# Kernel optimization log

Measured on AMD Instinct MI355X. Metric: run time of the kernel, lower is better.

## Reference

```python
import jax, jax.numpy as jnp
import numpy as np

N_NODES = 100000
N_EDGES = 1600000
IN = 128
HID = 128
OUT_CLS = 40
EPS = 1e-12


def setup_inputs() -> dict:
    key = jax.random.key(0)
    ks = jax.random.split(key, 12)
    feat = jax.random.normal(ks[0], (N_NODES, IN), dtype=jnp.float32)
    edge_index = jax.random.randint(ks[1], (2, N_EDGES), 0, N_NODES, dtype=jnp.int64)

    def xavier(k, shape):
        fan_out, fan_in = shape
        lim = float(np.sqrt(6.0 / (fan_in + fan_out)))
        return jax.random.uniform(k, shape, jnp.float32, -lim, lim)

    return {
        "feat": feat,
        "edge_index": edge_index,
        "Wl1": xavier(ks[2], (HID, IN)),  "bl1": jnp.zeros((HID,), jnp.float32), "Wr1": xavier(ks[3], (HID, IN)),
        "Wl2": xavier(ks[4], (HID, HID)), "bl2": jnp.zeros((HID,), jnp.float32), "Wr2": xavier(ks[5], (HID, HID)),
        "Wl3": xavier(ks[6], (HID, HID)), "bl3": jnp.zeros((HID,), jnp.float32), "Wr3": xavier(ks[7], (HID, HID)),
        "Wfc": xavier(ks[8], (OUT_CLS, HID)), "bfc": jnp.zeros((OUT_CLS,), jnp.float32),
    }


def sage_conv(x, src, dst, Wl, bl, Wr):
    # mean-aggregate neighbor messages x[src] into dst nodes (PyG aggr='mean')
    agg = jax.ops.segment_sum(x[src], dst, num_segments=N_NODES)        # [N, d]
    cnt = jax.ops.segment_sum(jnp.ones((src.shape[0],), x.dtype), dst,
                              num_segments=N_NODES)                      # [N]
    agg = agg / jnp.maximum(cnt, 1.0)[:, None]
    out = agg @ Wl.T + bl + x @ Wr.T                                     # lin_l(agg) + lin_r(x)
    # F.normalize(p=2, dim=-1, eps=1e-12)
    norm = jnp.linalg.norm(out, axis=-1, keepdims=True)
    return out / jnp.maximum(norm, EPS)


def reference(feat, edge_index, Wl1, bl1, Wr1, Wl2, bl2, Wr2, Wl3, bl3, Wr3, Wfc, bfc):
    src, dst = edge_index[0], edge_index[1]
    h = jax.nn.relu(sage_conv(feat, src, dst, Wl1, bl1, Wr1))
    h = jax.nn.relu(sage_conv(h, src, dst, Wl2, bl2, Wr2))
    h = sage_conv(h, src, dst, Wl3, bl3, Wr3)
    logits = h @ Wfc.T + bfc
    return jax.nn.softmax(logits, axis=-1)
```

## Files before the change

### kernel.cpp

```cpp
#include <hip/hip_runtime.h>
#include <cstdint>

#define N_NODES 100000
#define N_EDGES 1600000
#define F 128
#define OUT_CLS 40
#define LW 13
#define LBM (LW * 32)
#define BSHIFT 10
#define NBUCK 98
#define TILE 2048

using f32x16 = __attribute__((ext_vector_type(16))) float;
using bf16x8 = __attribute__((ext_vector_type(8))) short;
using f16x2 = __attribute__((ext_vector_type(2))) _Float16;
using f16x8 = __attribute__((ext_vector_type(8))) _Float16;

__device__ __forceinline__ int edge_val(const int* eb, int is64, long idx) {
  return is64 ? eb[2 * idx] : eb[idx];
}

__global__ void k_detect(const unsigned int* eb, int* flag) {
  if (threadIdx.x == 0 && blockIdx.x == 0) {
    int is64 = 1;
#pragma unroll
    for (int i = 1; i < 16; i += 2) is64 &= (eb[i] == 0u);
    flag[0] = is64;
  }
}

#define CH_E 16
__global__ __launch_bounds__(256) void k_chist(const int* __restrict__ eb, const int* __restrict__ flag,
                                               int* __restrict__ bhist) {
  __shared__ int lh[NBUCK];
  int t = threadIdx.x;
  if (t < NBUCK) lh[t] = 0;
  __syncthreads();
  int is64 = flag[0];
  long base = (long)blockIdx.x * (256 * CH_E);
#pragma unroll
  for (int i = 0; i < CH_E; ++i) {
    long e = base + (long)i * 256 + t;
    if (e < N_EDGES) {
      int d = edge_val(eb, is64, (long)N_EDGES + e);
      atomicAdd(&lh[d >> BSHIFT], 1);
    }
  }
  __syncthreads();
  if (t < NBUCK && lh[t]) atomicAdd(&bhist[t], lh[t]);
}

__global__ __launch_bounds__(128) void k_bscan(const int* __restrict__ bhist, int* __restrict__ boff,
                                               int* __restrict__ bkt_cursor, int* __restrict__ off) {
  __shared__ int sh[128];
  int t = threadIdx.x;
  int v = (t < NBUCK) ? bhist[t] : 0;
  sh[t] = v;
  __syncthreads();
  for (int d = 1; d < 128; d <<= 1) {
    int u = (t >= d) ? sh[t - d] : 0;
    __syncthreads();
    sh[t] += u;
    __syncthreads();
  }
  int incl = sh[t];
  if (t < NBUCK) {
    boff[t] = incl - v;
    bkt_cursor[t] = incl - v;
  }
  if (t == NBUCK - 1) boff[NBUCK] = incl;
  if (t == 0) off[N_NODES] = N_EDGES;
}

__global__ __launch_bounds__(256) void k_bscatter(const int* __restrict__ eb, const int* __restrict__ flag,
                                                  int* __restrict__ bkt_cursor, unsigned* __restrict__ ebuf) {
  __shared__ int lhist[128];
  __shared__ int lbase[128];
  __shared__ int gbase[NBUCK];
  __shared__ int lcnt[NBUCK];
  __shared__ unsigned buf[TILE];
  __shared__ int slotpos[TILE];
  int t = threadIdx.x;
  long e0 = (long)blockIdx.x * TILE;
  int is64 = flag[0];
  if (t < 128) lhist[t] = 0;
  __syncthreads();
#pragma unroll
  for (int i = 0; i < TILE / 256; ++i) {
    long e = e0 + t + i * 256;
    if (e < N_EDGES) {
      int d = edge_val(eb, is64, (long)N_EDGES + e);
      atomicAdd(&lhist[d >> BSHIFT], 1);
    }
  }
  __syncthreads();
  if (t < 128) lbase[t] = lhist[t];
  __syncthreads();
  for (int d = 1; d < 128; d <<= 1) {
    int v = (t >= d && t < 128) ? lbase[t - d] : 0;
    __syncthreads();
    if (t < 128) lbase[t] += v;
    __syncthreads();
  }
  if (t < NBUCK) {
    gbase[t] = atomicAdd(&bkt_cursor[t], lhist[t]);
    lcnt[t] = 0;
  }
  __syncthreads();
#pragma unroll
  for (int i = 0; i < TILE / 256; ++i) {
    long e = e0 + t + i * 256;
    if (e < N_EDGES) {
      int d = edge_val(eb, is64, (long)N_EDGES + e);
      int s = edge_val(eb, is64, e);
      int b = d >> BSHIFT;
      int n = atomicAdd(&lcnt[b], 1);
      int slot = lbase[b] - lhist[b] + n;
      buf[slot] = (unsigned)s | ((unsigned)(d & 1023) << 17);
      slotpos[slot] = gbase[b] + n;
    }
  }
  __syncthreads();
  int tile_n = (int)min((long)TILE, (long)N_EDGES - e0);
  for (int i = t; i < tile_n; i += 256) {
    ebuf[slotpos[i]] = buf[i];
  }
}

__global__ __launch_bounds__(1024) void k_fsort(const unsigned* __restrict__ ebuf, const int* __restrict__ boff,
                                                int* __restrict__ off, int* __restrict__ srcs) {
  __shared__ int hist[1024];
  __shared__ int cur[1024];
  __shared__ int wsum[16];
  int b = blockIdx.x;
  int t = threadIdx.x;
  int p0 = boff[b], p1 = boff[b + 1];
  hist[t] = 0;
  __syncthreads();
  for (int p = p0 + t; p < p1; p += 1024) {
    int d = (int)(ebuf[p] >> 17);
    atomicAdd(&hist[d], 1);
  }
  __syncthreads();
  int h = hist[t];
  int v = h;
#pragma unroll
  for (int o = 1; o < 64; o <<= 1) {
    int u = __shfl_up(v, o);
    if ((t & 63) >= o) v += u;
  }
  if ((t & 63) == 63) wsum[t >> 6] = v;
  __syncthreads();
  if (t < 64) {
    int w = (t < 16) ? wsum[t] : 0;
#pragma unroll
    for (int o = 1; o < 16; o <<= 1) {
      int u = __shfl_up(w, o);
      if (t >= o) w += u;
    }
    if (t < 16) wsum[t] = w;
  }
  __syncthreads();
  int base = (t >> 6) ? wsum[(t >> 6) - 1] : 0;
  int gpos = p0 + base + v - h;
  int node = (b << BSHIFT) + t;
  if (node < N_NODES) off[node] = gpos;
  cur[t] = gpos;
  __syncthreads();
  for (int p = p0 + t; p < p1; p += 1024) {
    unsigned e = ebuf[p];
    int pos = atomicAdd(&cur[(int)(e >> 17)], 1);
    srcs[pos] = (int)(e & 0x1FFFFu);
  }
}

__global__ __launch_bounds__(256) void k_tohalf(const float* __restrict__ in, _Float16* __restrict__ o) {
  int i = blockIdx.x * 256 + threadIdx.x;
  if (i >= N_NODES * F / 8) return;
  float4 a = reinterpret_cast<const float4*>(in)[2 * i];
  float4 b = reinterpret_cast<const float4*>(in)[2 * i + 1];
  union {
    _Float16 h[8];
    uint4 u;
  } r;
  r.h[0] = (_Float16)a.x; r.h[1] = (_Float16)a.y; r.h[2] = (_Float16)a.z; r.h[3] = (_Float16)a.w;
  r.h[4] = (_Float16)b.x; r.h[5] = (_Float16)b.y; r.h[6] = (_Float16)b.z; r.h[7] = (_Float16)b.w;
  reinterpret_cast<uint4*>(o)[i] = r.u;
}

__global__ __launch_bounds__(256) void k_aggregate(const _Float16* __restrict__ x, const int* __restrict__ off,
                                                   const int* __restrict__ srcs, float* __restrict__ agg) {
  int n = blockIdx.x * 4 + (threadIdx.x >> 6);
  if (n >= N_NODES) return;
  int l = threadIdx.x & 63;
  int p0 = off[n], p1 = off[n + 1];
  int deg = p1 - p0;
  float sx = 0.f, sy = 0.f;

  for (int base = 0; base < deg; base += 64) {
    int rem = deg - base;
    int cnt = (rem < 64) ? rem : 64;
    int my = (l < cnt) ? srcs[p0 + base + l] : 0;
    int j = 0;
    for (; j + 7 < cnt; j += 8) {
      int s[8];
#pragma unroll
      for (int k = 0; k < 8; ++k) s[k] = __builtin_amdgcn_readlane(my, j + k);
      f16x2 v[8];
#pragma unroll
      for (int k = 0; k < 8; ++k)
        v[k] = *reinterpret_cast<const f16x2*>(x + (size_t)(unsigned)s[k] * F + 2 * l);
#pragma unroll
      for (int k = 0; k < 8; ++k) {
        sx += (float)v[k][0];
        sy += (float)v[k][1];
      }
    }
    for (; j + 3 < cnt; j += 4) {
      int s[4];
#pragma unroll
      for (int k = 0; k < 4; ++k) s[k] = __builtin_amdgcn_readlane(my, j + k);
      f16x2 v[4];
#pragma unroll
      for (int k = 0; k < 4; ++k)
        v[k] = *reinterpret_cast<const f16x2*>(x + (size_t)(unsigned)s[k] * F + 2 * l);
#pragma unroll
      for (int k = 0; k < 4; ++k) {
        sx += (float)v[k][0];
        sy += (float)v[k][1];
      }
    }
    for (; j < cnt; ++j) {
      int s = __builtin_amdgcn_readlane(my, j);
      f16x2 v = *reinterpret_cast<const f16x2*>(x + (size_t)(unsigned)s * F + 2 * l);
      sx += (float)v[0];
      sy += (float)v[1];
    }
  }

  float inv = 1.0f / (float)max(deg, 1);
  float2 r;
  r.x = sx * inv;
  r.y = sy * inv;
  *reinterpret_cast<float2*>(agg + (size_t)n * F + 2 * l) = r;
}

__device__ __forceinline__ void split_pack(const float4& a, const float4& b, bf16x8& hi, bf16x8& lo) {
  float f[8] = {a.x, a.y, a.z, a.w, b.x, b.y, b.z, b.w};
#pragma unroll
  for (int i = 0; i < 8; ++i) {
    union { float f; unsigned u; } u0;
    u0.f = f[i];
    hi[i] = (short)(u0.u >> 16);
    union { unsigned u; float f; } uh;
    uh.u = u0.u & 0xFFFF0000u;
    union { float f; unsigned u; } ur;
    ur.f = f[i] - uh.f;
    lo[i] = (short)(ur.u >> 16);
  }
}

__device__ __forceinline__ void split_pack_h(const f16x8& v, bf16x8& hi, bf16x8& lo) {
#pragma unroll
  for (int i = 0; i < 8; ++i) {
    float f = (float)v[i];
    union { float f; unsigned u; } u0;
    u0.f = f;
    hi[i] = (short)(u0.u >> 16);
    union { unsigned u; float f; } uh;
    uh.u = u0.u & 0xFFFF0000u;
    union { float f; unsigned u; } ur;
    ur.f = f - uh.f;
    lo[i] = (short)(ur.u >> 16);
  }
}

__global__ __launch_bounds__(256) void k_wsplit(const float* __restrict__ Wl1, const float* __restrict__ Wr1,
                                                const float* __restrict__ Wl2, const float* __restrict__ Wr2,
                                                const float* __restrict__ Wl3, const float* __restrict__ Wr3,
                                                unsigned short* __restrict__ wsp) {
  int e = blockIdx.x * 256 + threadIdx.x;
  if (e >= 3 * 16384) return;
  int L = e >> 14, off = e & 16383;
  const float* wl = (L == 0) ? Wl1 : (L == 1) ? Wl2 : Wl3;
  const float* wr = (L == 0) ? Wr1 : (L == 1) ? Wr2 : Wr3;
  unsigned short* base = wsp + (size_t)L * 4 * 16384;
  {
    union { float f; unsigned u; } u0;
    u0.f = wl[off];
    union { unsigned u; float f; } uh;
    uh.u = u0.u & 0xFFFF0000u;
    union { float f; unsigned u; } ur;
    ur.f = u0.f - uh.f;
    base[off] = (unsigned short)(u0.u >> 16);
    base[16384 + off] = (unsigned short)(ur.u >> 16);
  }
  {
    union { float f; unsigned u; } u0;
    u0.f = wr[off];
    union { unsigned u; float f; } uh;
    uh.u = u0.u & 0xFFFF0000u;
    union { float f; unsigned u; } ur;
    ur.f = u0.f - uh.f;
    base[2 * 16384 + off] = (unsigned short)(u0.u >> 16);
    base[3 * 16384 + off] = (unsigned short)(ur.u >> 16);
  }
}

__global__ __launch_bounds__(832, 1) void k_linear(const float* __restrict__ agg, const _Float16* __restrict__ x16,
                                                   const unsigned short* __restrict__ wsp,
                                                   const float* __restrict__ bl, float* __restrict__ out,
                                                   _Float16* __restrict__ out16, int relu) {
  __shared__ unsigned short wlds[4][128][136];
  int tid = threadIdx.x;

  for (int c = tid; c < 4 * 2048; c += 832) {
    int m = c >> 11, rem = c & 2047;
    int j = rem >> 4, kc = (rem & 15) * 8;
    uint4 v = *reinterpret_cast<const uint4*>(wsp + (size_t)m * 16384 + j * 128 + kc);
    *reinterpret_cast<uint4*>(&wlds[m][j][kc]) = v;
  }
  __syncthreads();

  int wid = tid >> 6, lane = tid & 63;
  int l31 = lane & 31, lhi = lane >> 5;
  long rb = (long)blockIdx.x * LBM + (long)wid * 32;
  if (rb >= N_NODES) return;

  int r0 = (int)min(rb + l31, (long)N_NODES - 1);
  const float* a0p = agg + (size_t)r0 * F + lhi * 8;
  const _Float16* x0p = x16 + (size_t)r0 * F + lhi * 8;

  f32x16 acc[4];
#pragma unroll
  for (int ct = 0; ct < 4; ++ct) acc[ct] = (f32x16)0.f;

  float4 ap = *reinterpret_cast<const float4*>(a0p);
  float4 aq = *reinterpret_cast<const float4*>(a0p + 4);
  f16x8 xv = *reinterpret_cast<const f16x8*>(x0p);

#pragma unroll
  for (int ks = 0; ks < 8; ++ks) {
    float4 ap_n, aq_n;
    f16x8 xv_n;
    if (ks < 7) {
      const float* an = a0p + (ks + 1) * 16;
      ap_n = *reinterpret_cast<const float4*>(an);
      aq_n = *reinterpret_cast<const float4*>(an + 4);
      xv_n = *reinterpret_cast<const f16x8*>(x0p + (ks + 1) * 16);
    }
    int k0 = ks * 16 + lhi * 8;
    bf16x8 aH0, aL0, xH0, xL0;
    split_pack(ap, aq, aH0, aL0);
    split_pack_h(xv, xH0, xL0);
#pragma unroll
    for (int ct = 0; ct < 4; ++ct) {
      int j = ct * 32 + l31;
      bf16x8 BlH = *reinterpret_cast<const bf16x8*>(&wlds[0][j][k0]);
      bf16x8 BlL = *reinterpret_cast<const bf16x8*>(&wlds[1][j][k0]);
      bf16x8 BrH = *reinterpret_cast<const bf16x8*>(&wlds[2][j][k0]);
      bf16x8 BrL = *reinterpret_cast<const bf16x8*>(&wlds[3][j][k0]);
      acc[ct] = __builtin_amdgcn_mfma_f32_32x32x16_bf16(aH0, BlH, acc[ct], 0, 0, 0);
      acc[ct] = __builtin_amdgcn_mfma_f32_32x32x16_bf16(aL0, BlH, acc[ct], 0, 0, 0);
      acc[ct] = __builtin_amdgcn_mfma_f32_32x32x16_bf16(aH0, BlL, acc[ct], 0, 0, 0);
      acc[ct] = __builtin_amdgcn_mfma_f32_32x32x16_bf16(xH0, BrH, acc[ct], 0, 0, 0);
      acc[ct] = __builtin_amdgcn_mfma_f32_32x32x16_bf16(xL0, BrH, acc[ct], 0, 0, 0);
      acc[ct] = __builtin_amdgcn_mfma_f32_32x32x16_bf16(xH0, BrL, acc[ct], 0, 0, 0);
    }
    ap = ap_n;
    aq = aq_n;
    xv = xv_n;
  }

#pragma unroll
  for (int ct = 0; ct < 4; ++ct) {
    float b = bl[ct * 32 + l31];
#pragma unroll
    for (int i = 0; i < 16; ++i) acc[ct][i] += b;
  }
#pragma unroll
  for (int i = 0; i < 16; ++i) {
    float ss = acc[0][i] * acc[0][i] + acc[1][i] * acc[1][i] +
               acc[2][i] * acc[2][i] + acc[3][i] * acc[3][i];
#pragma unroll
    for (int o = 1; o < 32; o <<= 1) ss += __shfl_xor(ss, o);
    float inv = 1.0f / fmaxf(sqrtf(ss), 1e-12f);
    long grow = rb + (i & 3) + 8 * (i >> 2) + 4 * lhi;
    if (grow < N_NODES) {
      long base = grow * F + l31;
#pragma unroll
      for (int ct = 0; ct < 4; ++ct) {
        float v = acc[ct][i] * inv;
        if (relu) v = fmaxf(v, 0.f);
        if (out) out[base + ct * 32] = v;
        if (out16) out16[base + ct * 32] = (_Float16)v;
      }
    }
  }
}

#define FCP 132
__global__ __launch_bounds__(256) void k_fc_softmax(const float* __restrict__ h, const float* __restrict__ Wfc,
                                                    const float* __restrict__ bfc, float* __restrict__ out) {
  __shared__ float w_s[OUT_CLS][FCP];
  __shared__ float h_s[32][FCP];
  int tid = threadIdx.x;
  int nb = blockIdx.x * 32;

  for (int i = tid; i < OUT_CLS * (F / 4); i += 256) {
    int r = i >> 5, c = (i & 31) * 4;
    *reinterpret_cast<float4*>(&w_s[r][c]) = *reinterpret_cast<const float4*>(Wfc + (size_t)r * F + c);
  }
  for (int i = tid; i < 32 * (F / 4); i += 256) {
    int r = i >> 5, c = (i & 31) * 4;
    *reinterpret_cast<float4*>(&h_s[r][c]) = *reinterpret_cast<const float4*>(h + (size_t)(nb + r) * F + c);
  }
  __syncthreads();

  int r = tid >> 3, sub = tid & 7;
  float acc[5];
#pragma unroll
  for (int c = 0; c < 5; ++c) acc[c] = bfc[sub * 5 + c];

  for (int k4 = 0; k4 < F / 4; ++k4) {
    float4 hv = *reinterpret_cast<const float4*>(&h_s[r][k4 * 4]);
#pragma unroll
    for (int c = 0; c < 5; ++c) {
      float4 wv = *reinterpret_cast<const float4*>(&w_s[sub * 5 + c][k4 * 4]);
      acc[c] += hv.x * wv.x + hv.y * wv.y + hv.z * wv.z + hv.w * wv.w;
    }
  }

  float m = acc[0];
#pragma unroll
  for (int c = 1; c < 5; ++c) m = fmaxf(m, acc[c]);
#pragma unroll
  for (int o = 4; o > 0; o >>= 1) m = fmaxf(m, __shfl_xor(m, o));
  float e[5], s = 0.f;
#pragma unroll
  for (int c = 0; c < 5; ++c) {
    e[c] = expf(acc[c] - m);
    s += e[c];
  }
#pragma unroll
  for (int o = 4; o > 0; o >>= 1) s += __shfl_xor(s, o);
  float inv = 1.0f / s;
#pragma unroll
  for (int c = 0; c < 5; ++c) out[(size_t)(nb + r) * OUT_CLS + sub * 5 + c] = e[c] * inv;
}

extern "C" void kernel_launch(void* const* d_in, const int* in_sizes, int n_in, void* d_out, int out_size,
                              void* d_ws, size_t ws_size, hipStream_t stream) {
  const float* feat = (const float*)d_in[0];
  const int* eb = (const int*)d_in[1];
  const float* Wl1 = (const float*)d_in[2];
  const float* bl1 = (const float*)d_in[3];
  const float* Wr1 = (const float*)d_in[4];
  const float* Wl2 = (const float*)d_in[5];
  const float* bl2 = (const float*)d_in[6];
  const float* Wr2 = (const float*)d_in[7];
  const float* Wl3 = (const float*)d_in[8];
  const float* bl3 = (const float*)d_in[9];
  const float* Wr3 = (const float*)d_in[10];
  const float* Wfc = (const float*)d_in[11];
  const float* bfc = (const float*)d_in[12];
  float* out = (float*)d_out;

  char* w = (char*)d_ws;
  auto alloc = [&](size_t bytes) {
    char* p = w;
    w += (bytes + 255) & ~(size_t)255;
    return p;
  };
  int* flag = (int*)alloc(4);
  int* bhist = (int*)alloc((size_t)NBUCK * 4);
  int* boff = (int*)alloc((size_t)(NBUCK + 1) * 4);
  int* off = (int*)alloc((size_t)(N_NODES + 1) * 4);
  int* srcs = (int*)alloc((size_t)N_EDGES * 4 + 256);
  int* bkt_cursor = (int*)alloc((size_t)NBUCK * 4);
  unsigned short* wsp = (unsigned short*)alloc((size_t)3 * 4 * 16384 * 2);
  float* bufA = (float*)alloc((size_t)N_NODES * F * 4);
  float* bufB = (float*)alloc((size_t)N_NODES * F * 4);
  _Float16* h16X = (_Float16*)alloc((size_t)N_NODES * F * 2);
  _Float16* h16A = (_Float16*)alloc((size_t)N_NODES * F * 2);
  unsigned* ebuf = (unsigned*)bufB;
  (void)ws_size;
  (void)in_sizes;
  (void)n_in;
  (void)out_size;

  hipMemsetAsync(bhist, 0, (size_t)NBUCK * 4, stream);
  k_detect<<<1, 64, 0, stream>>>((const unsigned int*)eb, flag);
  k_chist<<<(N_EDGES + 256 * CH_E - 1) / (256 * CH_E), 256, 0, stream>>>(eb, flag, bhist);
  k_bscan<<<1, 128, 0, stream>>>(bhist, boff, bkt_cursor, off);
  k_bscatter<<<(N_EDGES + TILE - 1) / TILE, 256, 0, stream>>>(eb, flag, bkt_cursor, ebuf);
  k_fsort<<<NBUCK, 1024, 0, stream>>>(ebuf, boff, off, srcs);
  k_wsplit<<<192, 256, 0, stream>>>(Wl1, Wr1, Wl2, Wr2, Wl3, Wr3, wsp);
  k_tohalf<<<(N_NODES * F / 8 + 255) / 256, 256, 0, stream>>>(feat, h16X);

  const int nag = (N_NODES + 3) / 4;
  const int nlin = (N_NODES + LBM - 1) / LBM;
  const int nfc = N_NODES / 32;

  k_aggregate<<<nag, 256, 0, stream>>>(h16X, off, srcs, bufA);
  k_linear<<<nlin, 832, 0, stream>>>(bufA, h16X, wsp + 0 * 4 * 16384, bl1, ((float*)0), h16A, 1);
  k_aggregate<<<nag, 256, 0, stream>>>(h16A, off, srcs, bufB);
  k_linear<<<nlin, 832, 0, stream>>>(bufB, h16A, wsp + 1 * 4 * 16384, bl2, ((float*)0), h16X, 1);
  k_aggregate<<<nag, 256, 0, stream>>>(h16X, off, srcs, bufA);
  k_linear<<<nlin, 832, 0, stream>>>(bufA, h16X, wsp + 2 * 4 * 16384, bl3, bufB, ((_Float16*)0), 0);
  k_fc_softmax<<<nfc, 256, 0, stream>>>(bufB, Wfc, bfc, out);
}
```

Baseline: 395.6 us.

## Drop edge histogram pass via fixed-capacity buckets; store aggregates in fp16

The edge bucket sort now scatters into fixed-capacity per-bucket segments (ECAP entries each), so the separate count-histogram and scan kernels are removed and a scan runs on the final cursors instead. The aggregation kernel writes its mean result as fp16 rather than fp32, which halves that intermediate's write and read traffic in the linear kernel. The linear kernel now splits fp16 inputs for both operands. Risks: a bucket overflows if more than ECAP edges land in it, and the aggregate loses precision by being rounded to fp16.

```diff
diff --git a/kernel.cpp b/kernel.cpp
--- a/kernel.cpp
+++ b/kernel.cpp
@@ -10,6 +10,7 @@
 #define BSHIFT 10
 #define NBUCK 98
 #define TILE 2048
+#define ECAP 24576
 
 using f32x16 = __attribute__((ext_vector_type(16))) float;
 using bf16x8 = __attribute__((ext_vector_type(8))) short;
@@ -27,49 +28,6 @@
     for (int i = 1; i < 16; i += 2) is64 &= (eb[i] == 0u);
     flag[0] = is64;
   }
-}
-
-#define CH_E 16
-__global__ __launch_bounds__(256) void k_chist(const int* __restrict__ eb, const int* __restrict__ flag,
-                                               int* __restrict__ bhist) {
-  __shared__ int lh[NBUCK];
-  int t = threadIdx.x;
-  if (t < NBUCK) lh[t] = 0;
-  __syncthreads();
-  int is64 = flag[0];
-  long base = (long)blockIdx.x * (256 * CH_E);
-#pragma unroll
-  for (int i = 0; i < CH_E; ++i) {
-    long e = base + (long)i * 256 + t;
-    if (e < N_EDGES) {
-      int d = edge_val(eb, is64, (long)N_EDGES + e);
-      atomicAdd(&lh[d >> BSHIFT], 1);
-    }
-  }
-  __syncthreads();
-  if (t < NBUCK && lh[t]) atomicAdd(&bhist[t], lh[t]);
-}
-
-__global__ __launch_bounds__(128) void k_bscan(const int* __restrict__ bhist, int* __restrict__ boff,
-                                               int* __restrict__ bkt_cursor, int* __restrict__ off) {
-  __shared__ int sh[128];
-  int t = threadIdx.x;
-  int v = (t < NBUCK) ? bhist[t] : 0;
-  sh[t] = v;
-  __syncthreads();
-  for (int d = 1; d < 128; d <<= 1) {
-    int u = (t >= d) ? sh[t - d] : 0;
-    __syncthreads();
-    sh[t] += u;
-    __syncthreads();
-  }
-  int incl = sh[t];
-  if (t < NBUCK) {
-    boff[t] = incl - v;
-    bkt_cursor[t] = incl - v;
-  }
-  if (t == NBUCK - 1) boff[NBUCK] = incl;
-  if (t == 0) off[N_NODES] = N_EDGES;
 }
 
 __global__ __launch_bounds__(256) void k_bscatter(const int* __restrict__ eb, const int* __restrict__ flag,
@@ -117,7 +75,7 @@
       int n = atomicAdd(&lcnt[b], 1);
       int slot = lbase[b] - lhist[b] + n;
       buf[slot] = (unsigned)s | ((unsigned)(d & 1023) << 17);
-      slotpos[slot] = gbase[b] + n;
+      slotpos[slot] = b * ECAP + gbase[b] + n;
     }
   }
   __syncthreads();
@@ -125,6 +83,25 @@
   for (int i = t; i < tile_n; i += 256) {
     ebuf[slotpos[i]] = buf[i];
   }
+}
+
+__global__ __launch_bounds__(128) void k_bscan2(const int* __restrict__ bkt_cursor, int* __restrict__ boff,
+                                                int* __restrict__ off) {
+  __shared__ int sh[128];
+  int t = threadIdx.x;
+  int v = (t < NBUCK) ? bkt_cursor[t] : 0;
+  sh[t] = v;
+  __syncthreads();
+  for (int d = 1; d < 128; d <<= 1) {
+    int u = (t >= d) ? sh[t - d] : 0;
+    __syncthreads();
+    sh[t] += u;
+    __syncthreads();
+  }
+  int incl = sh[t];
+  if (t < NBUCK) boff[t] = incl - v;
+  if (t == NBUCK - 1) boff[NBUCK] = incl;
+  if (t == 0) off[N_NODES] = N_EDGES;
 }
 
 __global__ __launch_bounds__(1024) void k_fsort(const unsigned* __restrict__ ebuf, const int* __restrict__ boff,
@@ -135,10 +112,12 @@
   int b = blockIdx.x;
   int t = threadIdx.x;
   int p0 = boff[b], p1 = boff[b + 1];
+  int cnt = p1 - p0;
+  const unsigned* seg = ebuf + (size_t)b * ECAP;
   hist[t] = 0;
   __syncthreads();
-  for (int p = p0 + t; p < p1; p += 1024) {
-    int d = (int)(ebuf[p] >> 17);
+  for (int p = t; p < cnt; p += 1024) {
+    int d = (int)(seg[p] >> 17);
     atomicAdd(&hist[d], 1);
   }
   __syncthreads();
@@ -167,8 +146,8 @@
   if (node < N_NODES) off[node] = gpos;
   cur[t] = gpos;
   __syncthreads();
-  for (int p = p0 + t; p < p1; p += 1024) {
-    unsigned e = ebuf[p];
+  for (int p = t; p < cnt; p += 1024) {
+    unsigned e = seg[p];
     int pos = atomicAdd(&cur[(int)(e >> 17)], 1);
     srcs[pos] = (int)(e & 0x1FFFFu);
   }
@@ -189,7 +168,7 @@
 }
 
 __global__ __launch_bounds__(256) void k_aggregate(const _Float16* __restrict__ x, const int* __restrict__ off,
-                                                   const int* __restrict__ srcs, float* __restrict__ agg) {
+                                                   const int* __restrict__ srcs, _Float16* __restrict__ agg16) {
   int n = blockIdx.x * 4 + (threadIdx.x >> 6);
   if (n >= N_NODES) return;
   int l = threadIdx.x & 63;
@@ -239,25 +218,10 @@
   }
 
   float inv = 1.0f / (float)max(deg, 1);
-  float2 r;
-  r.x = sx * inv;
-  r.y = sy * inv;
-  *reinterpret_cast<float2*>(agg + (size_t)n * F + 2 * l) = r;
-}
-
-__device__ __forceinline__ void split_pack(const float4& a, const float4& b, bf16x8& hi, bf16x8& lo) {
-  float f[8] = {a.x, a.y, a.z, a.w, b.x, b.y, b.z, b.w};
-#pragma unroll
-  for (int i = 0; i < 8; ++i) {
-    union { float f; unsigned u; } u0;
-    u0.f = f[i];
-    hi[i] = (short)(u0.u >> 16);
-    union { unsigned u; float f; } uh;
-    uh.u = u0.u & 0xFFFF0000u;
-    union { float f; unsigned u; } ur;
-    ur.f = f[i] - uh.f;
-    lo[i] = (short)(ur.u >> 16);
-  }
+  f16x2 r;
+  r[0] = (_Float16)(sx * inv);
+  r[1] = (_Float16)(sy * inv);
+  *reinterpret_cast<f16x2*>(agg16 + (size_t)n * F + 2 * l) = r;
 }
 
 __device__ __forceinline__ void split_pack_h(const f16x8& v, bf16x8& hi, bf16x8& lo) {
@@ -307,7 +271,8 @@
   }
 }
 
-__global__ __launch_bounds__(832, 1) void k_linear(const float* __restrict__ agg, const _Float16* __restrict__ x16,
+__global__ __launch_bounds__(832, 1) void k_linear(const _Float16* __restrict__ agg16,
+                                                   const _Float16* __restrict__ x16,
                                                    const unsigned short* __restrict__ wsp,
                                                    const float* __restrict__ bl, float* __restrict__ out,
                                                    _Float16* __restrict__ out16, int relu) {
@@ -328,30 +293,26 @@
   if (rb >= N_NODES) return;
 
   int r0 = (int)min(rb + l31, (long)N_NODES - 1);
-  const float* a0p = agg + (size_t)r0 * F + lhi * 8;
+  const _Float16* a0p = agg16 + (size_t)r0 * F + lhi * 8;
   const _Float16* x0p = x16 + (size_t)r0 * F + lhi * 8;
 
   f32x16 acc[4];
 #pragma unroll
   for (int ct = 0; ct < 4; ++ct) acc[ct] = (f32x16)0.f;
 
-  float4 ap = *reinterpret_cast<const float4*>(a0p);
-  float4 aq = *reinterpret_cast<const float4*>(a0p + 4);
+  f16x8 av = *reinterpret_cast<const f16x8*>(a0p);
   f16x8 xv = *reinterpret_cast<const f16x8*>(x0p);
 
 #pragma unroll
   for (int ks = 0; ks < 8; ++ks) {
-    float4 ap_n, aq_n;
-    f16x8 xv_n;
+    f16x8 av_n, xv_n;
     if (ks < 7) {
-      const float* an = a0p + (ks + 1) * 16;
-      ap_n = *reinterpret_cast<const float4*>(an);
-      aq_n = *reinterpret_cast<const float4*>(an + 4);
+      av_n = *reinterpret_cast<const f16x8*>(a0p + (ks + 1) * 16);
       xv_n = *reinterpret_cast<const f16x8*>(x0p + (ks + 1) * 16);
     }
     int k0 = ks * 16 + lhi * 8;
     bf16x8 aH0, aL0, xH0, xL0;
-    split_pack(ap, aq, aH0, aL0);
+    split_pack_h(av, aH0, aL0);
     split_pack_h(xv, xH0, xL0);
 #pragma unroll
     for (int ct = 0; ct < 4; ++ct) {
@@ -367,8 +328,7 @@
       acc[ct] = __builtin_amdgcn_mfma_f32_32x32x16_bf16(xL0, BrH, acc[ct], 0, 0, 0);
       acc[ct] = __builtin_amdgcn_mfma_f32_32x32x16_bf16(xH0, BrL, acc[ct], 0, 0, 0);
     }
-    ap = ap_n;
-    aq = aq_n;
+    av = av_n;
     xv = xv_n;
   }
 
@@ -473,14 +433,13 @@
     return p;
   };
   int* flag = (int*)alloc(4);
-  int* bhist = (int*)alloc((size_t)NBUCK * 4);
   int* boff = (int*)alloc((size_t)(NBUCK + 1) * 4);
   int* off = (int*)alloc((size_t)(N_NODES + 1) * 4);
   int* srcs = (int*)alloc((size_t)N_EDGES * 4 + 256);
   int* bkt_cursor = (int*)alloc((size_t)NBUCK * 4);
   unsigned short* wsp = (unsigned short*)alloc((size_t)3 * 4 * 16384 * 2);
-  float* bufA = (float*)alloc((size_t)N_NODES * F * 4);
   float* bufB = (float*)alloc((size_t)N_NODES * F * 4);
+  _Float16* agg16 = (_Float16*)alloc((size_t)N_NODES * F * 2);
   _Float16* h16X = (_Float16*)alloc((size_t)N_NODES * F * 2);
   _Float16* h16A = (_Float16*)alloc((size_t)N_NODES * F * 2);
   unsigned* ebuf = (unsigned*)bufB;
@@ -489,11 +448,10 @@
   (void)n_in;
   (void)out_size;
 
-  hipMemsetAsync(bhist, 0, (size_t)NBUCK * 4, stream);
+  hipMemsetAsync(bkt_cursor, 0, (size_t)NBUCK * 4, stream);
   k_detect<<<1, 64, 0, stream>>>((const unsigned int*)eb, flag);
-  k_chist<<<(N_EDGES + 256 * CH_E - 1) / (256 * CH_E), 256, 0, stream>>>(eb, flag, bhist);
-  k_bscan<<<1, 128, 0, stream>>>(bhist, boff, bkt_cursor, off);
   k_bscatter<<<(N_EDGES + TILE - 1) / TILE, 256, 0, stream>>>(eb, flag, bkt_cursor, ebuf);
+  k_bscan2<<<1, 128, 0, stream>>>(bkt_cursor, boff, off);
   k_fsort<<<NBUCK, 1024, 0, stream>>>(ebuf, boff, off, srcs);
   k_wsplit<<<192, 256, 0, stream>>>(Wl1, Wr1, Wl2, Wr2, Wl3, Wr3, wsp);
   k_tohalf<<<(N_NODES * F / 8 + 255) / 256, 256, 0, stream>>>(feat, h16X);
@@ -502,11 +460,11 @@
   const int nlin = (N_NODES + LBM - 1) / LBM;
   const int nfc = N_NODES / 32;
 
-  k_aggregate<<<nag, 256, 0, stream>>>(h16X, off, srcs, bufA);
-  k_linear<<<nlin, 832, 0, stream>>>(bufA, h16X, wsp + 0 * 4 * 16384, bl1, ((float*)0), h16A, 1);
-  k_aggregate<<<nag, 256, 0, stream>>>(h16A, off, srcs, bufB);
-  k_linear<<<nlin, 832, 0, stream>>>(bufB, h16A, wsp + 1 * 4 * 16384, bl2, ((float*)0), h16X, 1);
-  k_aggregate<<<nag, 256, 0, stream>>>(h16X, off, srcs, bufA);
-  k_linear<<<nlin, 832, 0, stream>>>(bufA, h16X, wsp + 2 * 4 * 16384, bl3, bufB, ((_Float16*)0), 0);
+  k_aggregate<<<nag, 256, 0, stream>>>(h16X, off, srcs, agg16);
+  k_linear<<<nlin, 832, 0, stream>>>(agg16, h16X, wsp + 0 * 4 * 16384, bl1, ((float*)0), h16A, 1);
+  k_aggregate<<<nag, 256, 0, stream>>>(h16A, off, srcs, agg16);
+  k_linear<<<nlin, 832, 0, stream>>>(agg16, h16A, wsp + 1 * 4 * 16384, bl2, ((float*)0), h16X, 1);
+  k_aggregate<<<nag, 256, 0, stream>>>(h16X, off, srcs, agg16);
+  k_linear<<<nlin, 832, 0, stream>>>(agg16, h16X, wsp + 2 * 4 * 16384, bl3, bufB, ((_Float16*)0), 0);
   k_fc_softmax<<<nfc, 256, 0, stream>>>(bufB, Wfc, bfc, out);
 }
```

Result: faster. 369.2 us (-6.7%).
